# Optimization experiments

Measured on AMD Instinct MI355X. Metric: run time of the kernel, lower is better.

## Reference

```python
import jax, jax.numpy as jnp
import numpy as np

N, S, C, E = 32768, 32768, 1024, 16384   # nodes, subgraph-node entries, clusters (=B*P), coarsen edges
F, D, B, P, NC = 64, 64, 16, 64, 10      # feat dim, hidden, graphs, patches per graph, classes


def setup_inputs():
    key = jax.random.key(0)
    ks = list(jax.random.split(key, 24))
    p = lambda k, shp: jax.random.normal(k, shp, dtype=jnp.float32) * 0.05
    z = lambda n: jnp.zeros((n,), jnp.float32)
    return {
        "x": jax.random.normal(ks[0], (N, F), dtype=jnp.float32),
        "subgraphs_nodes_mapper": jax.random.randint(ks[1], (S,), 0, N, dtype=jnp.int32),
        "subgraphs_batch": jnp.sort(jax.random.randint(ks[2], (S,), 0, C, dtype=jnp.int32)),
        "subgraphs_batch_row": jax.random.randint(ks[3], (E,), 0, C, dtype=jnp.int32),
        "subgraphs_batch_col": jax.random.randint(ks[4], (E,), 0, C, dtype=jnp.int32),
        "coarsen_edge_attr": jax.random.uniform(ks[5], (E,), dtype=jnp.float32),
        "W_in1": p(ks[6], (F, D)), "b_in1": z(D),
        "W_in2": p(ks[7], (D, D)), "b_in2": z(D),
        "W_pre1": p(ks[8], (D, D)), "b_pre1": z(D),
        "W_pre2": p(ks[9], (D, D)), "b_pre2": z(D),
        "W_post1": p(ks[10], (D, D)), "b_post1": z(D),
        "W_post2": p(ks[11], (D, D)), "b_post2": z(D),
        "W_K": p(ks[12], (D, D)), "b_K": z(D),
        "W_V": p(ks[13], (D, D)), "b_V": z(D),
        "alpha_beta": jax.random.normal(ks[14], (2,), dtype=jnp.float32),
        "W_c1": p(ks[15], (D, D // 2)), "b_c1": z(D // 2),
        "W_c2": p(ks[16], (D // 2, NC)), "b_c2": z(NC),
    }


def reference(x, subgraphs_nodes_mapper, subgraphs_batch, subgraphs_batch_row,
              subgraphs_batch_col, coarsen_edge_attr,
              W_in1, b_in1, W_in2, b_in2, W_pre1, b_pre1, W_pre2, b_pre2,
              W_post1, b_post1, W_post2, b_post2, W_K, b_K, W_V, b_V,
              alpha_beta, W_c1, b_c1, W_c2, b_c2):
    seg_sum = lambda v, idx: jax.ops.segment_sum(v, idx, num_segments=C)
    # input transform MLP (use_gnn=False path)
    h = jax.nn.relu(x @ W_in1 + b_in1)
    h = jax.nn.relu(h @ W_in2 + b_in2)
    sx = h[subgraphs_nodes_mapper]                        # [S, D] irregular gather
    b = subgraphs_batch
    row, col = subgraphs_batch_row, subgraphs_batch_col
    # bincount-based symmetric degree normalization of coarsened edge weights
    deg = seg_sum(coarsen_edge_attr, row)                 # [C]
    dinv = jnp.where(deg > 0, deg ** -0.5, 0.0)
    ea = dinv[row] * coarsen_edge_attr * dinv[col]        # [E]
    # Q path: pre-deepset -> scatter sum -> post-deepset
    Q = jax.nn.relu(sx @ W_pre1 + b_pre1) @ W_pre2 + b_pre2
    Qs = seg_sum(Q, b)
    Qs = jax.nn.relu(Qs @ W_post1 + b_post1) @ W_post2 + b_post2  # [C, D]
    # K / V paths
    K = sx @ W_K + b_K                                    # [S, D]
    cnt = jnp.maximum(seg_sum(jnp.ones((S,), sx.dtype), b), 1.0)
    Ks = seg_sum(K, b) / cnt[:, None]                     # scatter-mean [C, D]
    V = sx @ W_V + b_V                                    # [S, D]
    # relu kernelization
    Qk, Kk, Ksk = jax.nn.relu(Qs), jax.nn.relu(K), jax.nn.relu(Ks)
    ab = jax.nn.softmax(alpha_beta)
    sa, sb = ab[0] ** -0.5, ab[1] ** -0.5
    ck = jnp.concatenate([sa * Ksk[b], sb * Kk], axis=-1)   # [S, 2D]
    cq = jnp.concatenate([sa * Qk, sb * Qk], axis=-1)       # [C, 2D] (diffQ=False)
    ck_s = seg_sum(ck, b)                                   # [C, 2D]
    M = ck[:, :, None] * V[:, None, :]                      # [S, 2D, D] per-entry outer product
    Ms = seg_sum(M, b)                                      # [C, 2D, D]
    # Double_Level_MessageProp / KeyProp on coarsened graph: out[c] = sum_e ea_e * x[row_e] at col_e
    Ms = seg_sum(ea[:, None, None] * Ms[row], col)
    ck_s = seg_sum(ea[:, None] * ck_s[row], col)
    H = jnp.einsum('ci,cij->cj', cq, Ms)                    # [C, D]
    den = jnp.sum(cq * ck_s, axis=-1, keepdims=True) + 1e-6
    out = H / den                                           # [C, D]
    g = out.reshape(B, P, D).mean(axis=1)                   # mean readout over patches
    logits = jax.nn.relu(g @ W_c1 + b_c1) @ W_c2 + b_c2     # [B, NC]
    return logits
```

## Files before the change

### kernel.cpp

```cpp
#include <hip/hip_runtime.h>
#include <math.h>

constexpr int NN = 32768;
constexpr int SS = 32768;
constexpr int CC = 1024;
constexpr int EE = 16384;
constexpr int BB = 16;
constexpr int PP = 64;
constexpr int NC = 10;
constexpr int ECAP = 64;

__device__ __forceinline__ float rdlane(float v, int l) {
    return __int_as_float(__builtin_amdgcn_readlane(__float_as_int(v), l));
}

#define TS 68

__device__ __forceinline__ void gemm64(const float* A, const float* W,
                                       const float* __restrict__ bias,
                                       int r0, int c0, float acc[4][4])
{
#pragma unroll
    for (int dc = 0; dc < 4; ++dc) {
        float bv = bias[c0 + dc];
        acc[0][dc] = bv; acc[1][dc] = bv; acc[2][dc] = bv; acc[3][dc] = bv;
    }
#pragma unroll 16
    for (int k = 0; k < 64; ++k) {
        float4 av = *(const float4*)(A + k * TS + r0);
        float4 wv = *(const float4*)(W + k * TS + c0);
        acc[0][0] = fmaf(av.x, wv.x, acc[0][0]); acc[0][1] = fmaf(av.x, wv.y, acc[0][1]);
        acc[0][2] = fmaf(av.x, wv.z, acc[0][2]); acc[0][3] = fmaf(av.x, wv.w, acc[0][3]);
        acc[1][0] = fmaf(av.y, wv.x, acc[1][0]); acc[1][1] = fmaf(av.y, wv.y, acc[1][1]);
        acc[1][2] = fmaf(av.y, wv.z, acc[1][2]); acc[1][3] = fmaf(av.y, wv.w, acc[1][3]);
        acc[2][0] = fmaf(av.z, wv.x, acc[2][0]); acc[2][1] = fmaf(av.z, wv.y, acc[2][1]);
        acc[2][2] = fmaf(av.z, wv.z, acc[2][2]); acc[2][3] = fmaf(av.z, wv.w, acc[2][3]);
        acc[3][0] = fmaf(av.w, wv.x, acc[3][0]); acc[3][1] = fmaf(av.w, wv.y, acc[3][1]);
        acc[3][2] = fmaf(av.w, wv.z, acc[3][2]); acc[3][3] = fmaf(av.w, wv.w, acc[3][3]);
    }
}

__device__ __forceinline__ void gemm64x3(const float* A, const float* Wa,
                                         const float* Wb, const float* Wc_,
                                         const float* __restrict__ b1_,
                                         const float* __restrict__ b2_,
                                         const float* __restrict__ b3_,
                                         int r0, int c0,
                                         float a1_[4][4], float a2_[4][4], float a3_[4][4])
{
#pragma unroll
    for (int dc = 0; dc < 4; ++dc) {
        float v1 = b1_[c0 + dc], v2 = b2_[c0 + dc], v3 = b3_[c0 + dc];
#pragma unroll
        for (int dr = 0; dr < 4; ++dr) { a1_[dr][dc] = v1; a2_[dr][dc] = v2; a3_[dr][dc] = v3; }
    }
#pragma unroll 4
    for (int k = 0; k < 64; ++k) {
        float4 av = *(const float4*)(A + k * TS + r0);
        float4 w1 = *(const float4*)(Wa + k * TS + c0);
        float4 w2 = *(const float4*)(Wb + k * TS + c0);
        float4 w3 = *(const float4*)(Wc_ + k * TS + c0);
        float ar[4] = {av.x, av.y, av.z, av.w};
        float u1[4] = {w1.x, w1.y, w1.z, w1.w};
        float u2[4] = {w2.x, w2.y, w2.z, w2.w};
        float u3[4] = {w3.x, w3.y, w3.z, w3.w};
#pragma unroll
        for (int dr = 0; dr < 4; ++dr)
#pragma unroll
            for (int dc = 0; dc < 4; ++dc) {
                a1_[dr][dc] = fmaf(ar[dr], u1[dc], a1_[dr][dc]);
                a2_[dr][dc] = fmaf(ar[dr], u2[dc], a2_[dr][dc]);
                a3_[dr][dc] = fmaf(ar[dr], u3[dc], a3_[dr][dc]);
            }
    }
}

__device__ __forceinline__ void writeW(float* dst, int tid,
                                       float4 a, float4 b, float4 c, float4 d)
{
    int colq = (tid & 15) * 4;
    int rb = tid >> 4;
    *(float4*)(dst + (rb     ) * TS + colq) = a;
    *(float4*)(dst + (rb + 16) * TS + colq) = b;
    *(float4*)(dst + (rb + 32) * TS + colq) = c;
    *(float4*)(dst + (rb + 48) * TS + colq) = d;
}

__device__ __forceinline__ void writeXT(float* dst, int tid,
                                        float4 a, float4 b, float4 c, float4 d)
{
    int rb = (tid * 4) & 63;
    int cb = tid >> 4;
    dst[(rb + 0) * TS + cb     ] = a.x;
    dst[(rb + 1) * TS + cb     ] = a.y;
    dst[(rb + 2) * TS + cb     ] = a.z;
    dst[(rb + 3) * TS + cb     ] = a.w;
    dst[(rb + 0) * TS + cb + 16] = b.x;
    dst[(rb + 1) * TS + cb + 16] = b.y;
    dst[(rb + 2) * TS + cb + 16] = b.z;
    dst[(rb + 3) * TS + cb + 16] = b.w;
    dst[(rb + 0) * TS + cb + 32] = c.x;
    dst[(rb + 1) * TS + cb + 32] = c.y;
    dst[(rb + 2) * TS + cb + 32] = c.z;
    dst[(rb + 3) * TS + cb + 32] = c.w;
    dst[(rb + 0) * TS + cb + 48] = d.x;
    dst[(rb + 1) * TS + cb + 48] = d.y;
    dst[(rb + 2) * TS + cb + 48] = d.z;
    dst[(rb + 3) * TS + cb + 48] = d.w;
}

__device__ __forceinline__ void outT_relu(float* dst, int r0, int c0, float acc[4][4])
{
#pragma unroll
    for (int dc = 0; dc < 4; ++dc) {
        *(float4*)(dst + (c0 + dc) * TS + r0) =
            make_float4(fmaxf(acc[0][dc], 0.f), fmaxf(acc[1][dc], 0.f),
                        fmaxf(acc[2][dc], 0.f), fmaxf(acc[3][dc], 0.f));
    }
}

__device__ __forceinline__ void outG2(float* __restrict__ dst, size_t rowbase, int ld,
                                      int off, int r0, int c0, float acc[4][4], bool dorelu)
{
#pragma unroll
    for (int dr = 0; dr < 4; ++dr) {
        float4 v = make_float4(acc[dr][0], acc[dr][1], acc[dr][2], acc[dr][3]);
        if (dorelu) {
            v.x = fmaxf(v.x, 0.f); v.y = fmaxf(v.y, 0.f);
            v.z = fmaxf(v.z, 0.f); v.w = fmaxf(v.w, 0.f);
        }
        *(float4*)(dst + (rowbase + r0 + dr) * ld + off + c0) = v;
    }
}

__global__ __launch_bounds__(256, 2) void k_node(
    const float* __restrict__ x,
    const int* __restrict__ row, const float* __restrict__ attr,
    const int* __restrict__ batch,
    const float* __restrict__ W1, const float* __restrict__ b1,
    const float* __restrict__ W2, const float* __restrict__ b2,
    const float* __restrict__ Wp1, const float* __restrict__ bp1,
    const float* __restrict__ WK, const float* __restrict__ bK,
    const float* __restrict__ WV, const float* __restrict__ bV,
    float* __restrict__ u, float* __restrict__ KV,
    float* __restrict__ deg, int* __restrict__ segoff,
    int* __restrict__ gcnt, int* __restrict__ ebuck,
    float* __restrict__ zbase)
{
    __shared__ __align__(16) float bufA[64 * TS];
    __shared__ __align__(16) float bufB[64 * TS];
    __shared__ __align__(16) float w0[64 * TS];
    __shared__ __align__(16) float w1[64 * TS];
    __shared__ float ldeg[16];
    __shared__ int lbk[4];
    int tid = threadIdx.x;
    int b = blockIdx.x;
    if (tid < 33) {
        int i = b * 33 + tid;
        if (i < 16640) ((float4*)zbase)[i] = make_float4(0.f, 0.f, 0.f, 0.f);
    }
    if (b < 64) {
        if (tid < 16) ldeg[tid] = 0.f;
        __syncthreads();
        int lo = b * 16;
#pragma unroll 4
        for (int i = 0; i < 64; ++i) {
            int e = i * 256 + tid;
            int r = row[e];
            unsigned d = (unsigned)(r - lo);
            if (d < 16u) atomicAdd(&ldeg[d], attr[e]);
        }
        __syncthreads();
        if (tid < 16) deg[lo + tid] = ldeg[tid];
    } else if (b < 192) {
        int t = (b - 64) * 256 + tid;
        int cur = batch[t];
        int prev = (t == 0) ? -1 : batch[t - 1];
        for (int c = prev + 1; c <= cur; ++c) segoff[c] = t;
        if (t == SS - 1)
            for (int c = cur + 1; c <= CC; ++c) segoff[c] = SS;
    } else if (b < 448) {
        int crow = (b - 192) * 4;
        if (tid < 4) lbk[tid] = 0;
        __syncthreads();
#pragma unroll 4
        for (int i = 0; i < 64; ++i) {
            int e = i * 256 + tid;
            int r = row[e];
            unsigned d = (unsigned)(r - crow);
            if (d < 4u) {
                int pos = atomicAdd(&lbk[d], 1);
                if (pos < ECAP) ebuck[(size_t)(crow + d) * ECAP + pos] = e;
            }
        }
        __syncthreads();
        if (tid < 4) gcnt[crow + tid] = min(lbk[tid], ECAP);
    }
    int tx = tid & 15, ty = tid >> 4;
    int r0 = ty * 4, c0 = tx * 4;
    size_t rowbase = (size_t)b * 64;
    const float* xb = x + rowbase * 64;
    float4 a0 = ((const float4*)W1)[tid];
    float4 a1 = ((const float4*)W1)[tid + 256];
    float4 a2 = ((const float4*)W1)[tid + 512];
    float4 a3 = ((const float4*)W1)[tid + 768];
    float4 x0 = ((const float4*)xb)[tid];
    float4 x1 = ((const float4*)xb)[tid + 256];
    float4 x2 = ((const float4*)xb)[tid + 512];
    float4 x3 = ((const float4*)xb)[tid + 768];
    writeW(w0, tid, a0, a1, a2, a3);
    writeXT(bufA, tid, x0, x1, x2, x3);
    __syncthreads();
    float acc[4][4];
    a0 = ((const float4*)W2)[tid];
    a1 = ((const float4*)W2)[tid + 256];
    a2 = ((const float4*)W2)[tid + 512];
    a3 = ((const float4*)W2)[tid + 768];
    gemm64(bufA, w0, b1, r0, c0, acc);
    outT_relu(bufB, r0, c0, acc);
    writeW(w1, tid, a0, a1, a2, a3);
    __syncthreads();
    a0 = ((const float4*)Wp1)[tid];
    a1 = ((const float4*)Wp1)[tid + 256];
    a2 = ((const float4*)Wp1)[tid + 512];
    a3 = ((const float4*)Wp1)[tid + 768];
    float4 k0 = ((const float4*)WK)[tid];
    float4 k1 = ((const float4*)WK)[tid + 256];
    float4 k2 = ((const float4*)WK)[tid + 512];
    float4 k3 = ((const float4*)WK)[tid + 768];
    float4 v0 = ((const float4*)WV)[tid];
    float4 v1 = ((const float4*)WV)[tid + 256];
    float4 v2 = ((const float4*)WV)[tid + 512];
    float4 v3 = ((const float4*)WV)[tid + 768];
    gemm64(bufB, w1, b2, r0, c0, acc);
    outT_relu(bufA, r0, c0, acc);
    writeW(w0, tid, a0, a1, a2, a3);
    writeW(w1, tid, k0, k1, k2, k3);
    writeW(bufB, tid, v0, v1, v2, v3);
    __syncthreads();
    float accU[4][4], accK[4][4], accV[4][4];
    gemm64x3(bufA, w0, w1, bufB, bp1, bK, bV, r0, c0, accU, accK, accV);
    outG2(u, rowbase, 64, 0, r0, c0, accU, true);
    outG2(KV, rowbase, 128, 0, r0, c0, accK, false);
    outG2(KV, rowbase, 128, 64, r0, c0, accV, false);
}

__global__ __launch_bounds__(256, 4) void k_qk(
    const float* __restrict__ u, const int* __restrict__ mapper,
    const int* __restrict__ segoff,
    const float* __restrict__ Wp2, const float* __restrict__ bp2,
    const float* __restrict__ Wpo1, const float* __restrict__ bpo1,
    const float* __restrict__ Wpo2, const float* __restrict__ bpo2,
    float* __restrict__ Qk)
{
    __shared__ float accs[4][64];
    int c = blockIdx.x;
    int tid = threadIdx.x, j = tid & 63, g = tid >> 6;
    int s0 = segoff[c], s1 = segoff[c + 1];
    float L = (float)(s1 - s0);
    if (tid < 64) {
        accs[0][tid] = 0.f;
        accs[1][tid] = L * bp2[tid];
        accs[2][tid] = bpo1[tid];
        accs[3][tid] = bpo2[tid];
    }
    __syncthreads();
    float us = 0.f;
    for (int s = s0 + g; s < s1; s += 4) us += u[(size_t)mapper[s] * 64 + j];
    atomicAdd(&accs[0][j], us);
    __syncthreads();
    float usv = accs[0][j];
    float p = 0.f;
#pragma unroll
    for (int t = 0; t < 16; ++t) {
        int i = g * 16 + t;
        p = fmaf(rdlane(usv, i), Wp2[i * 64 + j], p);
    }
    atomicAdd(&accs[1][j], p);
    __syncthreads();
    float qs = accs[1][j];
    p = 0.f;
#pragma unroll
    for (int t = 0; t < 16; ++t) {
        int i = g * 16 + t;
        p = fmaf(rdlane(qs, i), Wpo1[i * 64 + j], p);
    }
    atomicAdd(&accs[2][j], p);
    __syncthreads();
    float tv = fmaxf(accs[2][j], 0.f);
    p = 0.f;
#pragma unroll
    for (int t = 0; t < 16; ++t) {
        int i = g * 16 + t;
        p = fmaf(rdlane(tv, i), Wpo2[i * 64 + j], p);
    }
    atomicAdd(&accs[3][j], p);
    __syncthreads();
    if (g == 0) Qk[c * 64 + j] = fmaxf(accs[3][j], 0.f);
}

#define KSTR 72
#define MSTR 68

__global__ __launch_bounds__(256, 4) void k_msbedge(
    const float* __restrict__ KV, const int* __restrict__ mapper,
    const int* __restrict__ segoff, const float* __restrict__ Qk,
    const int* __restrict__ col, const float* __restrict__ attr,
    const float* __restrict__ deg,
    const int* __restrict__ gcnt, const int* __restrict__ ebuck,
    const float* __restrict__ ab,
    float* __restrict__ H, float* __restrict__ den)
{
    __shared__ __align__(16) float Kr[32 * KSTR];
    __shared__ __align__(16) float Vb[32 * KSTR];
    __shared__ __align__(16) float msb[64 * MSTR];
    __shared__ int map_lds[32];
    __shared__ float sums[192];
    __shared__ float dvec[64];
    __shared__ int ecol[ECAP];
    __shared__ float ewt[ECAP];
    int c = blockIdx.x;
    int tid = threadIdx.x, j = tid & 63, g = tid >> 6;
    int tx = tid & 15, ty = tid >> 4;
    int r0 = ty * 4, c0 = tx * 4;
    int ne = gcnt[c];
    if (ne == 0) return;
    int nr = (ne + 15) & ~15;
    if (tid < 192) sums[tid] = 0.f;
    if (tid < ne) {
        int e = ebuck[(size_t)c * ECAP + tid];
        int cd = col[e];
        float dc = deg[cd];
        float dinvc = dc > 0.f ? 1.f / sqrtf(dc) : 0.f;
        float drr = deg[c];
        float dinvr = drr > 0.f ? 1.f / sqrtf(drr) : 0.f;
        ecol[tid] = cd;
        ewt[tid] = dinvr * attr[e] * dinvc;
    }
    for (int p = ne + tid; p < nr; p += 256) { ecol[p] = c; ewt[p] = 0.f; }
    int s0 = segoff[c], s1 = segoff[c + 1];
    float acc[4][4];
#pragma unroll
    for (int a = 0; a < 4; ++a)
#pragma unroll
        for (int bq = 0; bq < 4; ++bq) acc[a][bq] = 0.f;
    float ks = 0.f, krs = 0.f, vs = 0.f;
    for (int sb = s0; sb < s1; sb += 32) {
        int clen = min(32, s1 - sb);
        __syncthreads();
        if (tid < clen) map_lds[tid] = mapper[sb + tid];
        __syncthreads();
        for (int p = tid; p < clen * 32; p += 256) {
            int e = p >> 5, q = p & 31;
            int m = map_lds[e];
            float4 v = *(const float4*)(KV + (size_t)m * 128 + q * 4);
            float* dst = (q < 16) ? &Kr[e * KSTR + q * 4] : &Vb[e * KSTR + (q - 16) * 4];
            *(float4*)dst = v;
        }
        __syncthreads();
#pragma unroll 4
        for (int s = 0; s < clen; ++s) {
            float4 a4 = *(const float4*)(&Kr[s * KSTR + r0]);
            float4 b4 = *(const float4*)(&Vb[s * KSTR + c0]);
            float ar0 = fmaxf(a4.x, 0.f), ar1 = fmaxf(a4.y, 0.f);
            float ar2 = fmaxf(a4.z, 0.f), ar3 = fmaxf(a4.w, 0.f);
            acc[0][0] = fmaf(ar0, b4.x, acc[0][0]); acc[0][1] = fmaf(ar0, b4.y, acc[0][1]);
            acc[0][2] = fmaf(ar0, b4.z, acc[0][2]); acc[0][3] = fmaf(ar0, b4.w, acc[0][3]);
            acc[1][0] = fmaf(ar1, b4.x, acc[1][0]); acc[1][1] = fmaf(ar1, b4.y, acc[1][1]);
            acc[1][2] = fmaf(ar1, b4.z, acc[1][2]); acc[1][3] = fmaf(ar1, b4.w, acc[1][3]);
            acc[2][0] = fmaf(ar2, b4.x, acc[2][0]); acc[2][1] = fmaf(ar2, b4.y, acc[2][1]);
            acc[2][2] = fmaf(ar2, b4.z, acc[2][2]); acc[2][3] = fmaf(ar2, b4.w, acc[2][3]);
            acc[3][0] = fmaf(ar3, b4.x, acc[3][0]); acc[3][1] = fmaf(ar3, b4.y, acc[3][1]);
            acc[3][2] = fmaf(ar3, b4.z, acc[3][2]); acc[3][3] = fmaf(ar3, b4.w, acc[3][3]);
        }
        for (int s = g; s < clen; s += 4) {
            float kv = Kr[s * KSTR + j];
            ks += kv;
            krs += fmaxf(kv, 0.f);
            vs += Vb[s * KSTR + j];
        }
    }
    atomicAdd(&sums[j], ks);
    atomicAdd(&sums[64 + j], krs);
    atomicAdd(&sums[128 + j], vs);
    __syncthreads();
    int L = s1 - s0;
    float Lr = (float)L;
    float invLm = 1.f / (float)(L > 0 ? L : 1);
    float a0 = ab[0], a1 = ab[1];
    float sa2 = 1.f + expf(a1 - a0);
    float sb2 = 1.f + expf(a0 - a1);
    if (tid < 64) {
        float kskv = fmaxf(sums[tid] * invLm, 0.f);
        dvec[tid] = sa2 * Lr * kskv + sb2 * sums[64 + tid];
    }
    float4 vsl4 = *(const float4*)(&sums[128 + c0]);
#pragma unroll
    for (int a = 0; a < 4; ++a) {
        float kska = fmaxf(sums[r0 + a] * invLm, 0.f) * sa2;
        *(float4*)(&msb[(r0 + a) * MSTR + c0]) =
            make_float4(fmaf(kska, vsl4.x, sb2 * acc[a][0]),
                        fmaf(kska, vsl4.y, sb2 * acc[a][1]),
                        fmaf(kska, vsl4.z, sb2 * acc[a][2]),
                        fmaf(kska, vsl4.w, sb2 * acc[a][3]));
    }
    __syncthreads();
    float dvreg = dvec[j];
    for (int m0 = g * 4; m0 < nr; m0 += 16) {
        int cd0 = ecol[m0 + 0], cd1 = ecol[m0 + 1];
        int cd2 = ecol[m0 + 2], cd3 = ecol[m0 + 3];
        float wt0 = ewt[m0 + 0], wt1 = ewt[m0 + 1];
        float wt2 = ewt[m0 + 2], wt3 = ewt[m0 + 3];
        float q0 = Qk[(size_t)cd0 * 64 + j];
        float q1 = Qk[(size_t)cd1 * 64 + j];
        float q2 = Qk[(size_t)cd2 * 64 + j];
        float q3 = Qk[(size_t)cd3 * 64 + j];
        float o0 = 0.f, o1 = 0.f, o2 = 0.f, o3 = 0.f;
#pragma unroll
        for (int i = 0; i < 64; ++i) {
            float mv = msb[i * MSTR + j];
            o0 = fmaf(rdlane(q0, i), mv, o0);
            o1 = fmaf(rdlane(q1, i), mv, o1);
            o2 = fmaf(rdlane(q2, i), mv, o2);
            o3 = fmaf(rdlane(q3, i), mv, o3);
        }
        float p0 = q0 * dvreg, p1 = q1 * dvreg, p2 = q2 * dvreg, p3 = q3 * dvreg;
#pragma unroll
        for (int o = 32; o > 0; o >>= 1) {
            p0 += __shfl_xor(p0, o);
            p1 += __shfl_xor(p1, o);
            p2 += __shfl_xor(p2, o);
            p3 += __shfl_xor(p3, o);
        }
        atomicAdd(&H[(size_t)cd0 * 64 + j], wt0 * o0);
        atomicAdd(&H[(size_t)cd1 * 64 + j], wt1 * o1);
        atomicAdd(&H[(size_t)cd2 * 64 + j], wt2 * o2);
        atomicAdd(&H[(size_t)cd3 * 64 + j], wt3 * o3);
        if (j == 0) {
            atomicAdd(&den[cd0], wt0 * p0);
            atomicAdd(&den[cd1], wt1 * p1);
            atomicAdd(&den[cd2], wt2 * p2);
            atomicAdd(&den[cd3], wt3 * p3);
        }
    }
}

__global__ __launch_bounds__(64) void k_final(
    const float* __restrict__ H, const float* __restrict__ den,
    const float* __restrict__ Wc1, const float* __restrict__ bc1,
    const float* __restrict__ Wc2, const float* __restrict__ bc2,
    float* __restrict__ out)
{
    int bg = blockIdx.x;
    int j = threadIdx.x;
    float acc = 0.f;
    for (int p = 0; p < PP; ++p) {
        int c = bg * PP + p;
        acc += H[c * 64 + j] / (den[c] + 1e-6f);
    }
    float g = acc * (1.f / (float)PP);
    int m = j & 31;
    float a1 = bc1[m];
#pragma unroll
    for (int i = 0; i < 64; ++i) a1 = fmaf(rdlane(g, i), Wc1[i * 32 + m], a1);
    float c1 = fmaxf(a1, 0.f);
    int n = (j < NC) ? j : 0;
    float a2 = bc2[n];
#pragma unroll
    for (int i = 0; i < 32; ++i) a2 = fmaf(rdlane(c1, i), Wc2[i * NC + n], a2);
    if (j < NC) out[bg * NC + j] = a2;
}

extern "C" void kernel_launch(void* const* d_in, const int* in_sizes, int n_in,
                              void* d_out, int out_size, void* d_ws, size_t ws_size,
                              hipStream_t stream)
{
    const float* x      = (const float*)d_in[0];
    const int*   mapper = (const int*)d_in[1];
    const int*   batch  = (const int*)d_in[2];
    const int*   row    = (const int*)d_in[3];
    const int*   col    = (const int*)d_in[4];
    const float* attr   = (const float*)d_in[5];
    const float* W_in1  = (const float*)d_in[6];
    const float* b_in1  = (const float*)d_in[7];
    const float* W_in2  = (const float*)d_in[8];
    const float* b_in2  = (const float*)d_in[9];
    const float* W_pre1 = (const float*)d_in[10];
    const float* b_pre1 = (const float*)d_in[11];
    const float* W_pre2 = (const float*)d_in[12];
    const float* b_pre2 = (const float*)d_in[13];
    const float* W_post1= (const float*)d_in[14];
    const float* b_post1= (const float*)d_in[15];
    const float* W_post2= (const float*)d_in[16];
    const float* b_post2= (const float*)d_in[17];
    const float* W_K    = (const float*)d_in[18];
    const float* b_K    = (const float*)d_in[19];
    const float* W_V    = (const float*)d_in[20];
    const float* b_V    = (const float*)d_in[21];
    const float* alpha_beta = (const float*)d_in[22];
    const float* W_c1   = (const float*)d_in[23];
    const float* b_c1   = (const float*)d_in[24];
    const float* W_c2   = (const float*)d_in[25];
    const float* b_c2   = (const float*)d_in[26];

    float* ws = (float*)d_ws;
    float* u     = ws;
    float* KV    = u     + (size_t)NN * 64;
    float* Qk    = KV    + (size_t)NN * 128;
    float* deg   = Qk    + (size_t)CC * 64;
    float* H     = deg   + (size_t)CC;
    float* den   = H     + (size_t)CC * 64;
    int*  segoff = (int*)(den + (size_t)CC);
    int*  gcnt   = segoff + (CC + 1);
    int*  ebuck  = gcnt + CC;

    k_node<<<NN / 64, 256, 0, stream>>>(x, row, attr, batch,
                                        W_in1, b_in1, W_in2, b_in2,
                                        W_pre1, b_pre1, W_K, b_K, W_V, b_V,
                                        u, KV, deg, segoff, gcnt, ebuck, H);
    k_qk<<<CC, 256, 0, stream>>>(u, mapper, segoff, W_pre2, b_pre2,
                                 W_post1, b_post1, W_post2, b_post2, Qk);
    k_msbedge<<<CC, 256, 0, stream>>>(KV, mapper, segoff, Qk, col, attr,
                                      deg, gcnt, ebuck, alpha_beta, H, den);
    k_final<<<BB, 64, 0, stream>>>(H, den, W_c1, b_c1, W_c2, b_c2, (float*)d_out);
}
```

Baseline: 89.94 us.

## Move edge bucketing to k_qk and software-prefetch gathers in qk and edge loops

Moves the per-row edge bucketing work (ebuck/gcnt) out of k_node into the first 256 blocks of k_qk, which shortens the critical-path blocks in k_node. It also adds one-step software prefetch to the u-gather loop in k_qk and to the Qk/ecol/ewt loads in the k_msbedge edge loop, so memory latency overlaps compute. This costs extra registers and adds load imbalance in k_qk, since the low-index blocks now do the bucketing scan as well.

Result: slower. 95.40 us (+6.1%).

```diff
diff --git a/kernel.cpp b/kernel.cpp
--- a/kernel.cpp
+++ b/kernel.cpp
@@ -144,7 +144,6 @@
     const float* __restrict__ WV, const float* __restrict__ bV,
     float* __restrict__ u, float* __restrict__ KV,
     float* __restrict__ deg, int* __restrict__ segoff,
-    int* __restrict__ gcnt, int* __restrict__ ebuck,
     float* __restrict__ zbase)
 {
     __shared__ __align__(16) float bufA[64 * TS];
@@ -152,7 +151,6 @@
     __shared__ __align__(16) float w0[64 * TS];
     __shared__ __align__(16) float w1[64 * TS];
     __shared__ float ldeg[16];
-    __shared__ int lbk[4];
     int tid = threadIdx.x;
     int b = blockIdx.x;
     if (tid < 33) {
@@ -179,22 +177,6 @@
         for (int c = prev + 1; c <= cur; ++c) segoff[c] = t;
         if (t == SS - 1)
             for (int c = cur + 1; c <= CC; ++c) segoff[c] = SS;
-    } else if (b < 448) {
-        int crow = (b - 192) * 4;
-        if (tid < 4) lbk[tid] = 0;
-        __syncthreads();
-#pragma unroll 4
-        for (int i = 0; i < 64; ++i) {
-            int e = i * 256 + tid;
-            int r = row[e];
-            unsigned d = (unsigned)(r - crow);
-            if (d < 4u) {
-                int pos = atomicAdd(&lbk[d], 1);
-                if (pos < ECAP) ebuck[(size_t)(crow + d) * ECAP + pos] = e;
-            }
-        }
-        __syncthreads();
-        if (tid < 4) gcnt[crow + tid] = min(lbk[tid], ECAP);
     }
     int tx = tid & 15, ty = tid >> 4;
     int r0 = ty * 4, c0 = tx * 4;
@@ -247,15 +229,33 @@
 
 __global__ __launch_bounds__(256, 4) void k_qk(
     const float* __restrict__ u, const int* __restrict__ mapper,
-    const int* __restrict__ segoff,
+    const int* __restrict__ segoff, const int* __restrict__ row,
     const float* __restrict__ Wp2, const float* __restrict__ bp2,
     const float* __restrict__ Wpo1, const float* __restrict__ bpo1,
     const float* __restrict__ Wpo2, const float* __restrict__ bpo2,
-    float* __restrict__ Qk)
+    float* __restrict__ Qk, int* __restrict__ gcnt, int* __restrict__ ebuck)
 {
     __shared__ float accs[4][64];
+    __shared__ int lbk[4];
     int c = blockIdx.x;
     int tid = threadIdx.x, j = tid & 63, g = tid >> 6;
+    if (c < 256) {
+        int crow = c * 4;
+        if (tid < 4) lbk[tid] = 0;
+        __syncthreads();
+#pragma unroll 4
+        for (int i = 0; i < 64; ++i) {
+            int e = i * 256 + tid;
+            int r = row[e];
+            unsigned d = (unsigned)(r - crow);
+            if (d < 4u) {
+                int pos = atomicAdd(&lbk[d], 1);
+                if (pos < ECAP) ebuck[(size_t)(crow + d) * ECAP + pos] = e;
+            }
+        }
+        __syncthreads();
+        if (tid < 4) gcnt[crow + tid] = min(lbk[tid], ECAP);
+    }
     int s0 = segoff[c], s1 = segoff[c + 1];
     float L = (float)(s1 - s0);
     if (tid < 64) {
@@ -266,7 +266,21 @@
     }
     __syncthreads();
     float us = 0.f;
-    for (int s = s0 + g; s < s1; s += 4) us += u[(size_t)mapper[s] * 64 + j];
+    {
+        int s = s0 + g;
+        if (s < s1) {
+            float uv = u[(size_t)mapper[s] * 64 + j];
+            for (;;) {
+                int s2 = s + 4;
+                float uv2 = 0.f;
+                if (s2 < s1) uv2 = u[(size_t)mapper[s2] * 64 + j];
+                us += uv;
+                if (s2 >= s1) break;
+                uv = uv2;
+                s = s2;
+            }
+        }
+    }
     atomicAdd(&accs[0][j], us);
     __syncthreads();
     float usv = accs[0][j];
@@ -406,15 +420,31 @@
     }
     __syncthreads();
     float dvreg = dvec[j];
-    for (int m0 = g * 4; m0 < nr; m0 += 16) {
-        int cd0 = ecol[m0 + 0], cd1 = ecol[m0 + 1];
-        int cd2 = ecol[m0 + 2], cd3 = ecol[m0 + 3];
-        float wt0 = ewt[m0 + 0], wt1 = ewt[m0 + 1];
-        float wt2 = ewt[m0 + 2], wt3 = ewt[m0 + 3];
-        float q0 = Qk[(size_t)cd0 * 64 + j];
-        float q1 = Qk[(size_t)cd1 * 64 + j];
-        float q2 = Qk[(size_t)cd2 * 64 + j];
-        float q3 = Qk[(size_t)cd3 * 64 + j];
+    int m0 = g * 4;
+    if (m0 >= nr) return;
+    int cd0 = ecol[m0 + 0], cd1 = ecol[m0 + 1];
+    int cd2 = ecol[m0 + 2], cd3 = ecol[m0 + 3];
+    float wt0 = ewt[m0 + 0], wt1 = ewt[m0 + 1];
+    float wt2 = ewt[m0 + 2], wt3 = ewt[m0 + 3];
+    float q0 = Qk[(size_t)cd0 * 64 + j];
+    float q1 = Qk[(size_t)cd1 * 64 + j];
+    float q2 = Qk[(size_t)cd2 * 64 + j];
+    float q3 = Qk[(size_t)cd3 * 64 + j];
+    for (; m0 < nr; ) {
+        int n0 = m0 + 16;
+        int ncd0 = 0, ncd1 = 0, ncd2 = 0, ncd3 = 0;
+        float nwt0 = 0.f, nwt1 = 0.f, nwt2 = 0.f, nwt3 = 0.f;
+        float nq0 = 0.f, nq1 = 0.f, nq2 = 0.f, nq3 = 0.f;
+        if (n0 < nr) {
+            ncd0 = ecol[n0 + 0]; ncd1 = ecol[n0 + 1];
+            ncd2 = ecol[n0 + 2]; ncd3 = ecol[n0 + 3];
+            nwt0 = ewt[n0 + 0]; nwt1 = ewt[n0 + 1];
+            nwt2 = ewt[n0 + 2]; nwt3 = ewt[n0 + 3];
+            nq0 = Qk[(size_t)ncd0 * 64 + j];
+            nq1 = Qk[(size_t)ncd1 * 64 + j];
+            nq2 = Qk[(size_t)ncd2 * 64 + j];
+            nq3 = Qk[(size_t)ncd3 * 64 + j];
+        }
         float o0 = 0.f, o1 = 0.f, o2 = 0.f, o3 = 0.f;
 #pragma unroll
         for (int i = 0; i < 64; ++i) {
@@ -442,6 +472,10 @@
             atomicAdd(&den[cd2], wt2 * p2);
             atomicAdd(&den[cd3], wt3 * p3);
         }
+        m0 = n0;
+        cd0 = ncd0; cd1 = ncd1; cd2 = ncd2; cd3 = ncd3;
+        wt0 = nwt0; wt1 = nwt1; wt2 = nwt2; wt3 = nwt3;
+        q0 = nq0; q1 = nq1; q2 = nq2; q3 = nq3;
     }
 }
 
@@ -517,9 +551,10 @@
     k_node<<<NN / 64, 256, 0, stream>>>(x, row, attr, batch,
                                         W_in1, b_in1, W_in2, b_in2,
                                         W_pre1, b_pre1, W_K, b_K, W_V, b_V,
-                                        u, KV, deg, segoff, gcnt, ebuck, H);
-    k_qk<<<CC, 256, 0, stream>>>(u, mapper, segoff, W_pre2, b_pre2,
-                                 W_post1, b_post1, W_post2, b_post2, Qk);
+                                        u, KV, deg, segoff, H);
+    k_qk<<<CC, 256, 0, stream>>>(u, mapper, segoff, row, W_pre2, b_pre2,
+                                 W_post1, b_post1, W_post2, b_post2,
+                                 Qk, gcnt, ebuck);
     k_msbedge<<<CC, 256, 0, stream>>>(KV, mapper, segoff, Qk, col, attr,
                                       deg, gcnt, ebuck, alpha_beta, H, den);
     k_final<<<BB, 64, 0, stream>>>(H, den, W_c1, b_c1, W_c2, b_c2, (float*)d_out);
```
